# Kernel tuning notes

Hardware: AMD Instinct MI355X
Metric: run time of the kernel (lower is better)

## Reference

```python
import jax, jax.numpy as jnp
import numpy as np

B, D, E, K = 8192, 768, 8, 32  # batch, hidden, n_main_intents, max sub-intents


def setup_inputs() -> dict:
    key = jax.random.key(0)
    k1, k2, k3, k4, k5 = jax.random.split(key, 5)
    pooled = jax.random.normal(k1, (B, D), dtype=jnp.float32)
    main_W = jax.random.normal(k2, (D, E), dtype=jnp.float32) * 0.02
    main_b = jax.random.normal(k3, (E,), dtype=jnp.float32) * 0.02
    sub_W = jax.random.normal(k4, (E, D, K), dtype=jnp.float32) * 0.02
    sub_b = jax.random.normal(k5, (E, K), dtype=jnp.float32) * 0.02
    # sub-classifier output sizes per main intent: 32,31,...,25 (from intent_structure)
    sub_sizes = (K - jnp.arange(E)).astype(jnp.int32)
    return {"pooled": pooled, "main_W": main_W, "main_b": main_b,
            "sub_W": sub_W, "sub_b": sub_b, "sub_sizes": sub_sizes}


def reference(pooled, main_W, main_b, sub_W, sub_b, sub_sizes):
    # Dropout(0.3) is identity in eval mode.
    main_out = pooled @ main_W + main_b                      # [B, E]
    idx = jnp.argmax(main_out, axis=1)                       # top-1 routing [B]
    Wg = jnp.take(sub_W, idx, axis=0)                        # gather [B, D, K]
    bg = jnp.take(sub_b, idx, axis=0)                        # [B, K]
    sub_out = jnp.einsum('bd,bdk->bk', pooled, Wg) + bg      # per-sample small GEMV
    # padded scatter: sub_outputs[i, :n_sub(idx_i)] = sub_out, rest stays zero
    valid = jnp.arange(K)[None, :] < jnp.take(sub_sizes, idx)[:, None]
    sub_out = jnp.where(valid, sub_out, jnp.zeros((), sub_out.dtype))
    return main_out, sub_out
```

## Files before the change

### kernel.cpp

```cpp
#include <hip/hip_runtime.h>

#define BB 8192
#define DD 768
#define EE 8
#define KK 32

typedef short    short8 __attribute__((ext_vector_type(8)));
typedef float    f32x4  __attribute__((ext_vector_type(4)));
typedef float    f32x8  __attribute__((ext_vector_type(8)));
typedef unsigned short us4 __attribute__((ext_vector_type(4)));

__device__ __forceinline__ unsigned short f2bf(float f) {
  unsigned int u = __float_as_uint(f);
  u = (u + 0x7fffu + ((u >> 16) & 1u)) >> 16;
  return (unsigned short)u;
}

__global__ __launch_bounds__(256) void pack_w(const float* __restrict__ sw,
                                              short* __restrict__ bp) {
  const int t  = blockIdx.x * 256 + threadIdx.x;
  const int d0 = (t % (DD / 8)) * 8;
  const int ek = t / (DD / 8);
  const int e  = ek >> 5;
  const int k  = ek & 31;
  const float* src = sw + ((size_t)e * DD + d0) * KK + k;
  short8 v;
#pragma unroll
  for (int j = 0; j < 8; ++j) v[j] = (short)f2bf(src[(size_t)j * KK]);
  *(short8*)(bp + (size_t)ek * DD + d0) = v;
}

__global__ __launch_bounds__(512) void fused(
    const float* __restrict__ pooled, const float* __restrict__ mW,
    const float* __restrict__ mb, const short* __restrict__ Bp,
    const float* __restrict__ sub_b, const int* __restrict__ sub_sizes,
    float* __restrict__ main_out, float* __restrict__ sub_out) {
  __shared__ short aS[32][776];
  __shared__ int   idxS[32];
  __shared__ int   szS[32];

  const int t    = threadIdx.x;
  const int w    = t >> 6;
  const int lane = t & 63;
  const int row0 = blockIdx.x * 32;

  f32x8 acc[4] = {};
#pragma unroll
  for (int i = 0; i < 3; ++i) {
    const int d = (i * 64 + lane) * 4;
    f32x8 W0 = *(const f32x8*)(mW + (size_t)(d + 0) * EE);
    f32x8 W1 = *(const f32x8*)(mW + (size_t)(d + 1) * EE);
    f32x8 W2 = *(const f32x8*)(mW + (size_t)(d + 2) * EE);
    f32x8 W3 = *(const f32x8*)(mW + (size_t)(d + 3) * EE);
#pragma unroll
    for (int rr = 0; rr < 4; ++rr) {
      const int r = w * 4 + rr;
      f32x4 v = *(const f32x4*)(pooled + (size_t)(row0 + r) * DD + d);
      us4 u;
      u[0] = f2bf(v[0]); u[1] = f2bf(v[1]); u[2] = f2bf(v[2]); u[3] = f2bf(v[3]);
      *(us4*)&aS[r][d] = u;
      acc[rr] += v[0] * W0;
      acc[rr] += v[1] * W1;
      acc[rr] += v[2] * W2;
      acc[rr] += v[3] * W3;
    }
  }
#pragma unroll
  for (int rr = 0; rr < 4; ++rr) {
#pragma unroll
    for (int off = 32; off >= 1; off >>= 1) {
#pragma unroll
      for (int j = 0; j < 8; ++j) acc[rr][j] += __shfl_xor(acc[rr][j], off);
    }
    if (lane == 0) {
      const int r = w * 4 + rr;
      f32x8 res = acc[rr] + *(const f32x8*)mb;
      *(f32x8*)(main_out + (size_t)(row0 + r) * EE) = res;
      float best = res[0];
      int   bi   = 0;
#pragma unroll
      for (int e = 1; e < EE; ++e) {
        if (res[e] > best) { best = res[e]; bi = e; }
      }
      idxS[r] = bi;
      szS[r]  = sub_sizes[bi];
    }
  }
  __syncthreads();

  const int lc = lane & 15, hi = lane >> 4;
  const short* bb  = Bp + (size_t)w * KK * DD + (size_t)hi * 8;
  const short* bp0 = bb + (size_t)(lc) * DD;
  const short* bp1 = bb + (size_t)(16 + lc) * DD;
  f32x4 a2[2][2] = {};

  for (int ks = 0; ks < DD / 32; ++ks) {
    const int d0 = ks * 32 + hi * 8;
    short8 b0 = *(const short8*)(bp0 + ks * 32);
    short8 b1 = *(const short8*)(bp1 + ks * 32);
    short8 a0 = *(const short8*)&aS[lc][d0];
    short8 a1 = *(const short8*)&aS[16 + lc][d0];
    a2[0][0] = __builtin_amdgcn_mfma_f32_16x16x32_bf16(a0, b0, a2[0][0], 0, 0, 0);
    a2[0][1] = __builtin_amdgcn_mfma_f32_16x16x32_bf16(a0, b1, a2[0][1], 0, 0, 0);
    a2[1][0] = __builtin_amdgcn_mfma_f32_16x16x32_bf16(a1, b0, a2[1][0], 0, 0, 0);
    a2[1][1] = __builtin_amdgcn_mfma_f32_16x16x32_bf16(a1, b1, a2[1][1], 0, 0, 0);
  }

#pragma unroll
  for (int n = 0; n < 2; ++n) {
    const int k = n * 16 + lc;
    const float bias = sub_b[w * KK + k];
#pragma unroll
    for (int mt = 0; mt < 2; ++mt) {
#pragma unroll
      for (int q = 0; q < 4; ++q) {
        const int rl = mt * 16 + hi * 4 + q;
        if (idxS[rl] == w) {
          float v = a2[mt][n][q] + bias;
          if (k >= szS[rl]) v = 0.f;
          sub_out[(size_t)(row0 + rl) * KK + k] = v;
        }
      }
    }
  }
}

extern "C" void kernel_launch(void* const* d_in, const int* in_sizes, int n_in,
                              void* d_out, int out_size, void* d_ws, size_t ws_size,
                              hipStream_t stream) {
  const float* pooled   = (const float*)d_in[0];
  const float* main_W   = (const float*)d_in[1];
  const float* main_b   = (const float*)d_in[2];
  const float* sub_W    = (const float*)d_in[3];
  const float* sub_b    = (const float*)d_in[4];
  const int*   sub_size = (const int*)d_in[5];

  float* main_out = (float*)d_out;
  float* sub_out  = (float*)d_out + (size_t)BB * EE;
  short* Bp       = (short*)d_ws;

  pack_w<<<(EE * KK * DD / 8) / 256, 256, 0, stream>>>(sub_W, Bp);
  fused<<<BB / 32, 512, 0, stream>>>(pooled, main_W, main_b, Bp, sub_b,
                                     sub_size, main_out, sub_out);
}
```

Baseline: 34.24 us.

## Split MFMA reduction dimension across two wave halves and remap pack_w threads

The fused kernel now launches 1024 threads per block. Each wave handles 2 rows for the main GEMV instead of 4, and each expert's sub-GEMM K-loop is split across two waves that are combined through shared memory. This doubles per-block parallelism and shortens the serial MFMA chain. The cost is an extra barrier, a shared-memory reduction and higher register pressure under the tighter launch bound. pack_w is also remapped so consecutive threads read consecutive k, which coalesces the global loads from sub_W.

```diff
diff --git a/kernel.cpp b/kernel.cpp
--- a/kernel.cpp
+++ b/kernel.cpp
@@ -19,18 +19,18 @@
 __global__ __launch_bounds__(256) void pack_w(const float* __restrict__ sw,
                                               short* __restrict__ bp) {
   const int t  = blockIdx.x * 256 + threadIdx.x;
-  const int d0 = (t % (DD / 8)) * 8;
-  const int ek = t / (DD / 8);
-  const int e  = ek >> 5;
-  const int k  = ek & 31;
-  const float* src = sw + ((size_t)e * DD + d0) * KK + k;
+  const int k  = t & 31;
+  const int g  = t >> 5;
+  const int d0 = (g % 96) * 8;
+  const int e  = g / 96;
+  const float* src = sw + ((size_t)(e * DD + d0)) * KK + k;
   short8 v;
 #pragma unroll
   for (int j = 0; j < 8; ++j) v[j] = (short)f2bf(src[(size_t)j * KK]);
-  *(short8*)(bp + (size_t)ek * DD + d0) = v;
+  *(short8*)(bp + ((size_t)(e * KK + k)) * DD + d0) = v;
 }
 
-__global__ __launch_bounds__(512) void fused(
+__global__ __launch_bounds__(1024) void fused(
     const float* __restrict__ pooled, const float* __restrict__ mW,
     const float* __restrict__ mb, const short* __restrict__ Bp,
     const float* __restrict__ sub_b, const int* __restrict__ sub_sizes,
@@ -44,7 +44,7 @@
   const int lane = t & 63;
   const int row0 = blockIdx.x * 32;
 
-  f32x8 acc[4] = {};
+  f32x8 acc[2] = {};
 #pragma unroll
   for (int i = 0; i < 3; ++i) {
     const int d = (i * 64 + lane) * 4;
@@ -53,8 +53,8 @@
     f32x8 W2 = *(const f32x8*)(mW + (size_t)(d + 2) * EE);
     f32x8 W3 = *(const f32x8*)(mW + (size_t)(d + 3) * EE);
 #pragma unroll
-    for (int rr = 0; rr < 4; ++rr) {
-      const int r = w * 4 + rr;
+    for (int rr = 0; rr < 2; ++rr) {
+      const int r = w * 2 + rr;
       f32x4 v = *(const f32x4*)(pooled + (size_t)(row0 + r) * DD + d);
       us4 u;
       u[0] = f2bf(v[0]); u[1] = f2bf(v[1]); u[2] = f2bf(v[2]); u[3] = f2bf(v[3]);
@@ -66,14 +66,14 @@
     }
   }
 #pragma unroll
-  for (int rr = 0; rr < 4; ++rr) {
+  for (int rr = 0; rr < 2; ++rr) {
 #pragma unroll
     for (int off = 32; off >= 1; off >>= 1) {
 #pragma unroll
       for (int j = 0; j < 8; ++j) acc[rr][j] += __shfl_xor(acc[rr][j], off);
     }
     if (lane == 0) {
-      const int r = w * 4 + rr;
+      const int r = w * 2 + rr;
       f32x8 res = acc[rr] + *(const f32x8*)mb;
       *(f32x8*)(main_out + (size_t)(row0 + r) * EE) = res;
       float best = res[0];
@@ -88,13 +88,18 @@
   }
   __syncthreads();
 
-  const int lc = lane & 15, hi = lane >> 4;
-  const short* bb  = Bp + (size_t)w * KK * DD + (size_t)hi * 8;
-  const short* bp0 = bb + (size_t)(lc) * DD;
+  const int e    = w & 7;
+  const int half = w >> 3;
+  const int lc   = lane & 15, hi = lane >> 4;
+  const short* bb  = Bp + (size_t)e * KK * DD + (size_t)hi * 8;
+  const short* bp0 = bb + (size_t)lc * DD;
   const short* bp1 = bb + (size_t)(16 + lc) * DD;
   f32x4 a2[2][2] = {};
+  const int ks0 = half * 12;
 
-  for (int ks = 0; ks < DD / 32; ++ks) {
+#pragma unroll
+  for (int ii = 0; ii < 12; ++ii) {
+    const int ks = ks0 + ii;
     const int d0 = ks * 32 + hi * 8;
     short8 b0 = *(const short8*)(bp0 + ks * 32);
     short8 b1 = *(const short8*)(bp1 + ks * 32);
@@ -105,20 +110,38 @@
     a2[1][0] = __builtin_amdgcn_mfma_f32_16x16x32_bf16(a1, b0, a2[1][0], 0, 0, 0);
     a2[1][1] = __builtin_amdgcn_mfma_f32_16x16x32_bf16(a1, b1, a2[1][1], 0, 0, 0);
   }
+  __syncthreads();
 
+  f32x4* red = (f32x4*)&aS[0][0];
+#define RI(ai) (((ai) * 8 + e) * 64 + lane)
+  if (half) {
+    red[RI(0)] = a2[0][0];
+    red[RI(1)] = a2[0][1];
+    red[RI(2)] = a2[1][0];
+    red[RI(3)] = a2[1][1];
+  }
+  __syncthreads();
+
+  if (!half) {
+    a2[0][0] += red[RI(0)];
+    a2[0][1] += red[RI(1)];
+    a2[1][0] += red[RI(2)];
+    a2[1][1] += red[RI(3)];
+#undef RI
 #pragma unroll
-  for (int n = 0; n < 2; ++n) {
-    const int k = n * 16 + lc;
-    const float bias = sub_b[w * KK + k];
+    for (int n = 0; n < 2; ++n) {
+      const int k = n * 16 + lc;
+      const float bias = sub_b[e * KK + k];
 #pragma unroll
-    for (int mt = 0; mt < 2; ++mt) {
+      for (int mt = 0; mt < 2; ++mt) {
 #pragma unroll
-      for (int q = 0; q < 4; ++q) {
-        const int rl = mt * 16 + hi * 4 + q;
-        if (idxS[rl] == w) {
-          float v = a2[mt][n][q] + bias;
-          if (k >= szS[rl]) v = 0.f;
-          sub_out[(size_t)(row0 + rl) * KK + k] = v;
+        for (int q = 0; q < 4; ++q) {
+          const int rl = mt * 16 + hi * 4 + q;
+          if (idxS[rl] == e) {
+            float v = a2[mt][n][q] + bias;
+            if (k >= szS[rl]) v = 0.f;
+            sub_out[(size_t)(row0 + rl) * KK + k] = v;
+          }
         }
       }
     }
@@ -140,6 +163,6 @@
   short* Bp       = (short*)d_ws;
 
   pack_w<<<(EE * KK * DD / 8) / 256, 256, 0, stream>>>(sub_W, Bp);
-  fused<<<BB / 32, 512, 0, stream>>>(pooled, main_W, main_b, Bp, sub_b,
-                                     sub_size, main_out, sub_out);
+  fused<<<BB / 32, 1024, 0, stream>>>(pooled, main_W, main_b, Bp, sub_b,
+                                      sub_size, main_out, sub_out);
 }
```

New measurement: 42.28 us. 1.23x slower.
